# Performance work log

Measured on AMD Instinct MI355X. Metric: run time of the kernel, lower is better.

The kernel has to match this reference:

```python
import jax, jax.numpy as jnp
import numpy as np

N_NODES = 100000
IN_DIM = 64
OUT_DIM = 64
N_EDGES = 1600000


def _undirected_self_loops(edge_index, num_nodes):
    """Symmetrize, add self loops, coalesce (dedup+sort) like the torch module.
    edge_index is an integer constant, so we preprocess with numpy (no grads flow here).
    Returns (src, dst, w) where w are symmetric GCN normalization weights.
    """
    ei = np.asarray(edge_index, dtype=np.int64)
    loops = np.arange(num_nodes, dtype=np.int64)
    full_src = np.concatenate([ei[0], ei[1], loops])
    full_dst = np.concatenate([ei[1], ei[0], loops])
    keys = np.unique(full_src * num_nodes + full_dst)  # coalesce, sorted
    src = keys // num_nodes
    dst = keys % num_nodes
    deg = np.bincount(dst, minlength=num_nodes).clip(min=1)
    inv_sqrt = deg.astype(np.float32) ** -0.5
    w = inv_sqrt[src] * inv_sqrt[dst]
    return src, dst, w


def setup_inputs() -> dict:
    key = jax.random.key(0)
    kx, kw, kb, ke = jax.random.split(key, 4)
    x = jax.random.normal(kx, (N_NODES, IN_DIM), dtype=jnp.float32)
    # nn.Linear params: W (out, in), b (out,)
    W = jax.random.normal(kw, (OUT_DIM, IN_DIM), dtype=jnp.float32) / np.sqrt(IN_DIM)
    b = jax.random.normal(kb, (OUT_DIM,), dtype=jnp.float32) * 0.01
    edge_index = jax.random.randint(ke, (2, N_EDGES), 0, N_NODES, dtype=jnp.int64)
    return {"x": x, "edge_index": edge_index, "W": W, "b": b}


def reference(x, edge_index, W, b) -> jnp.ndarray:
    n = x.shape[0]
    src_np, dst_np, w_np = _undirected_self_loops(edge_index, n)
    src = jnp.asarray(src_np)
    dst = jnp.asarray(dst_np)
    w = jnp.asarray(w_np).astype(x.dtype)  # (E',)
    h = x @ W.T + b                         # (N, out_dim)
    msg = h[src] * w[:, None]               # gather + per-edge scale, (E', out_dim)
    out = jnp.zeros_like(h).at[dst].add(msg)  # scatter-add aggregation
    return out
```

## Files before the change

### kernel.cpp

```cpp
#include <hip/hip_runtime.h>
#include <hip/hip_bf16.h>
#include <stdint.h>

#define NN 100000
#define EE 1600000
#define CAP 128
#define NB 782
#define CAPB 5120
#define HTS 8192
#define EMPTY 0xFFFFFFFFu
#define BCHUNK 2048
#define GBIN 782
#define GLIN 1563

typedef float  fx4 __attribute__((ext_vector_type(4)));

__device__ __forceinline__ unsigned int mix32(unsigned int x){
  x ^= x >> 16; x *= 0x7feb352du;
  x ^= x >> 15; x *= 0x846ca68bu;
  x ^= x >> 16;
  return x;
}

extern "C" __global__ __launch_bounds__(256)
void k_prep(const float* __restrict__ x, const float* __restrict__ W,
            const float* __restrict__ bias, __hip_bfloat16* __restrict__ hb,
            const int* __restrict__ ei, int* __restrict__ bcnt,
            unsigned int* __restrict__ bbuf){
  __shared__ __align__(16) char sm[17920];
  const int tid = threadIdx.x;
  const int bid = blockIdx.x;
  const bool isbin = (bid < GBIN);
  const int sub = isbin ? bid : (bid - GBIN);

  if (!isbin){
    __hip_bfloat16 (*wt)[72] = reinterpret_cast<__hip_bfloat16(*)[72]>(sm);
    __hip_bfloat16 (*xs)[68] = reinterpret_cast<__hip_bfloat16(*)[68]>(sm + 9216);
    const int lane = tid & 63;
    const int wv   = tid >> 6;
    #pragma unroll
    for (int r = 0; r < 16; ++r){
      int i = r*4 + wv;
      wt[i][lane] = __float2bfloat16(W[lane*64 + i]);
    }
    const int nbase = sub * 64;
    #pragma unroll
    for (int r = 0; r < 4; ++r){
      int idx = r*256 + tid;
      int nl  = idx >> 4;
      int c4  = idx & 15;
      int n   = nbase + nl;
      float4 v = make_float4(0.f,0.f,0.f,0.f);
      if (n < NN) v = reinterpret_cast<const float4*>(x)[(size_t)n*16 + c4];
      xs[c4*4+0][nl] = __float2bfloat16(v.x);
      xs[c4*4+1][nl] = __float2bfloat16(v.y);
      xs[c4*4+2][nl] = __float2bfloat16(v.z);
      xs[c4*4+3][nl] = __float2bfloat16(v.w);
    }
    __syncthreads();

    const int og  = tid & 7;
    const int nl0 = (tid >> 3) * 2;
    float acc[2][8];
    #pragma unroll
    for (int t=0;t<2;++t){
      #pragma unroll
      for (int j=0;j<8;++j) acc[t][j]=0.f;
    }
    #pragma unroll 4
    for (int i=0;i<64;++i){
      uint4 wq = *reinterpret_cast<const uint4*>(&wt[i][og*8]);
      float w0 = __uint_as_float(wq.x << 16), w1 = __uint_as_float(wq.x & 0xFFFF0000u);
      float w2 = __uint_as_float(wq.y << 16), w3 = __uint_as_float(wq.y & 0xFFFF0000u);
      float w4 = __uint_as_float(wq.z << 16), w5 = __uint_as_float(wq.z & 0xFFFF0000u);
      float w6 = __uint_as_float(wq.w << 16), w7 = __uint_as_float(wq.w & 0xFFFF0000u);
      unsigned xv = *reinterpret_cast<const unsigned*>(&xs[i][nl0]);
      float x0 = __uint_as_float(xv << 16);
      float x1 = __uint_as_float(xv & 0xFFFF0000u);
      acc[0][0] += x0*w0; acc[0][1] += x0*w1; acc[0][2] += x0*w2; acc[0][3] += x0*w3;
      acc[0][4] += x0*w4; acc[0][5] += x0*w5; acc[0][6] += x0*w6; acc[0][7] += x0*w7;
      acc[1][0] += x1*w0; acc[1][1] += x1*w1; acc[1][2] += x1*w2; acc[1][3] += x1*w3;
      acc[1][4] += x1*w4; acc[1][5] += x1*w5; acc[1][6] += x1*w6; acc[1][7] += x1*w7;
    }
    float4 b0 = reinterpret_cast<const float4*>(bias)[og*2];
    float4 b1 = reinterpret_cast<const float4*>(bias)[og*2+1];
    float bb[8] = {b0.x,b0.y,b0.z,b0.w,b1.x,b1.y,b1.z,b1.w};
    #pragma unroll
    for (int t=0;t<2;++t){
      int n = nbase + nl0 + t;
      if (n < NN){
        union { uint4 u4; __hip_bfloat16 v[8]; } pk;
        #pragma unroll
        for (int j=0;j<8;++j) pk.v[j] = __float2bfloat16(acc[t][j] + bb[j]);
        reinterpret_cast<uint4*>(&hb[(size_t)n*64])[og] = pk.u4;
      }
    }
  } else {
    int* bcur  = reinterpret_cast<int*>(sm);
    int* bbase = bcur + NB;
    for (int i = tid; i < NB; i += 256) bcur[i] = 0;
    __syncthreads();
    const int e0 = sub * BCHUNK;
    const int4* ea4 = reinterpret_cast<const int4*>(ei);
    const int4* ec4 = reinterpret_cast<const int4*>(ei + EE);
    int4 A0, C0, A1, C1;
    unsigned P[8];
    {
      int idx0 = (e0 >> 2) + tid;
      int idx1 = idx0 + 256;
      if (idx0*4 < EE){ A0 = ea4[idx0]; C0 = ec4[idx0]; }
      else { A0 = make_int4(-1,-1,-1,-1); C0 = A0; }
      if (idx1*4 < EE){ A1 = ea4[idx1]; C1 = ec4[idx1]; }
      else { A1 = make_int4(-1,-1,-1,-1); C1 = A1; }
    }
#define RESV(a,c,slot) \
    if ((a) >= 0){ \
      unsigned p1 = (unsigned)atomicAdd(&bcur[(c) >> 7], 1); \
      unsigned p2 = (unsigned)atomicAdd(&bcur[(a) >> 7], 1); \
      P[slot] = p1 | (p2 << 16); \
    }
    RESV(A0.x, C0.x, 0) RESV(A0.y, C0.y, 1) RESV(A0.z, C0.z, 2) RESV(A0.w, C0.w, 3)
    RESV(A1.x, C1.x, 4) RESV(A1.y, C1.y, 5) RESV(A1.z, C1.z, 6) RESV(A1.w, C1.w, 7)
#undef RESV
    __syncthreads();
    for (int bk = tid; bk < NB; bk += 256){
      int hh = bcur[bk];
      bbase[bk] = hh ? atomicAdd(&bcnt[bk], hh) : 0;
    }
    __syncthreads();
#define PLACE(a,c,slot) \
    if ((a) >= 0){ \
      int b1 = (c) >> 7, b2 = (a) >> 7; \
      unsigned q1 = (unsigned)bbase[b1] + (P[slot] & 0xFFFFu); \
      unsigned q2 = (unsigned)bbase[b2] + (P[slot] >> 16); \
      if (q1 < CAPB) bbuf[(size_t)b1*CAPB + q1] = ((unsigned)(a) << 7) | (unsigned)((c) & 127); \
      if (q2 < CAPB) bbuf[(size_t)b2*CAPB + q2] = ((unsigned)(c) << 7) | (unsigned)((a) & 127); \
    }
    PLACE(A0.x, C0.x, 0) PLACE(A0.y, C0.y, 1) PLACE(A0.z, C0.z, 2) PLACE(A0.w, C0.w, 3)
    PLACE(A1.x, C1.x, 4) PLACE(A1.y, C1.y, 5) PLACE(A1.z, C1.z, 6) PLACE(A1.w, C1.w, 7)
#undef PLACE
  }
}

extern "C" __global__ __launch_bounds__(256)
void k_dedup(const int* __restrict__ bcnt, const unsigned int* __restrict__ bbuf,
             unsigned int* __restrict__ srclist, int* __restrict__ cnt,
             float* __restrict__ inv){
  __shared__ unsigned int HT[HTS];
  __shared__ int dcur[128];
  const int tid = threadIdx.x;
  const int b   = blockIdx.x;
  const int d0  = b << 7;
  uint4* HT4 = reinterpret_cast<uint4*>(HT);
  #pragma unroll
  for (int r = 0; r < 8; ++r) HT4[r*256 + tid] = make_uint4(EMPTY,EMPTY,EMPTY,EMPTY);
  if (tid < 128) dcur[tid] = 0;
  __syncthreads();

  int n = bcnt[b]; if (n > CAPB) n = CAPB;
  const unsigned int* buf = bbuf + (size_t)b * CAPB;
  for (int k = tid; k < n; k += 256){
    unsigned int pk  = buf[k];
    unsigned int idx = mix32(pk) & (HTS-1);
    for (;;){
      unsigned int prev = atomicCAS(&HT[idx], EMPTY, pk);
      if (prev == EMPTY || prev == pk) break;
      idx = (idx + 1) & (HTS-1);
    }
  }
  if (tid < 128 && d0 + tid < NN){
    unsigned int pk  = ((unsigned)(d0 + tid) << 7) | (unsigned)tid;
    unsigned int idx = mix32(pk) & (HTS-1);
    for (;;){
      unsigned int prev = atomicCAS(&HT[idx], EMPTY, pk);
      if (prev == EMPTY || prev == pk) break;
      idx = (idx + 1) & (HTS-1);
    }
  }
  __syncthreads();

  for (int i = tid; i < HTS; i += 256){
    unsigned int v = HT[i];
    if (v != EMPTY){
      int dl  = v & 127;
      int pos = atomicAdd(&dcur[dl], 1);
      if (pos < CAP) srclist[(size_t)(d0 + dl) * CAP + pos] = v >> 7;
    }
  }
  __syncthreads();
  if (tid < 128 && d0 + tid < NN){
    int c = dcur[tid];
    cnt[d0 + tid] = c;
    inv[d0 + tid] = rsqrtf((float)c);
  }
}

extern "C" __global__ __launch_bounds__(256)
void k_agg(const __hip_bfloat16* __restrict__ hb, const float* __restrict__ inv,
           const int* __restrict__ cnt, const unsigned int* __restrict__ srclist,
           float* __restrict__ out){
  __shared__ uint2 sv[4][CAP];
  const int wv   = threadIdx.x >> 6;
  const int lane = threadIdx.x & 63;
  const int g    = lane >> 4;
  const int pl   = lane & 15;
  const int d    = blockIdx.x*4 + wv;
  if (d >= NN) return;
  const unsigned int* reg = srclist + (size_t)d * CAP;
  int c = cnt[d]; if (c > CAP) c = CAP;
  const int cp = (c + 15) & ~15;

  if (lane < c){
    unsigned s = __builtin_nontemporal_load(reg + lane);
    sv[wv][lane] = make_uint2(s, __float_as_uint(inv[s]));
  }
  if (64 + lane < c){
    unsigned s = __builtin_nontemporal_load(reg + 64 + lane);
    sv[wv][64 + lane] = make_uint2(s, __float_as_uint(inv[s]));
  }
  { int p = c + lane; if (p < cp) sv[wv][p] = make_uint2(0u, 0u); }

  const char* hbase = (const char*)hb;
  const int   boff  = pl << 3;
  float4 acc[4];
  #pragma unroll
  for (int u=0;u<4;++u) acc[u] = make_float4(0.f,0.f,0.f,0.f);
  #pragma unroll 2
  for (int j = 0; j < cp; j += 16){
    #pragma unroll
    for (int u = 0; u < 4; ++u){
      uint2 e = sv[wv][j + 4*u + g];
      float w = __uint_as_float(e.y);
      uint2 hv = *reinterpret_cast<const uint2*>(hbase + ((size_t)e.x << 7) + boff);
      acc[u].x += w * __uint_as_float(hv.x << 16);
      acc[u].y += w * __uint_as_float(hv.x & 0xFFFF0000u);
      acc[u].z += w * __uint_as_float(hv.y << 16);
      acc[u].w += w * __uint_as_float(hv.y & 0xFFFF0000u);
    }
  }
  float4 r;
  r.x = (acc[0].x+acc[1].x)+(acc[2].x+acc[3].x);
  r.y = (acc[0].y+acc[1].y)+(acc[2].y+acc[3].y);
  r.z = (acc[0].z+acc[1].z)+(acc[2].z+acc[3].z);
  r.w = (acc[0].w+acc[1].w)+(acc[2].w+acc[3].w);
  r.x += __shfl_xor(r.x, 16); r.y += __shfl_xor(r.y, 16);
  r.z += __shfl_xor(r.z, 16); r.w += __shfl_xor(r.w, 16);
  r.x += __shfl_xor(r.x, 32); r.y += __shfl_xor(r.y, 32);
  r.z += __shfl_xor(r.z, 32); r.w += __shfl_xor(r.w, 32);
  if (g == 0){
    float iv = inv[d];
    fx4 o; o.x = r.x*iv; o.y = r.y*iv; o.z = r.z*iv; o.w = r.w*iv;
    __builtin_nontemporal_store(o, reinterpret_cast<fx4*>(&out[(size_t)d*64]) + pl);
  }
}

extern "C" void kernel_launch(void* const* d_in, const int* in_sizes, int n_in,
                              void* d_out, int out_size, void* d_ws, size_t ws_size,
                              hipStream_t stream){
  (void)in_sizes; (void)n_in; (void)out_size; (void)ws_size;
  const float* x  = (const float*)d_in[0];
  const int*   ei = (const int*)  d_in[1];
  const float* W  = (const float*)d_in[2];
  const float* b  = (const float*)d_in[3];
  float* out = (float*)d_out;

  char* ws = (char*)d_ws;
  __hip_bfloat16* hb      = (__hip_bfloat16*)ws;
  float*          inv     = (float*)(ws + 12800000);
  int*            cnt     = (int*)  (ws + 13200000);
  unsigned int*   srclist = (unsigned int*)(ws + 13600000);
  int*            bcnt    = (int*)  (ws + 64800000);
  unsigned int*   bbuf    = (unsigned int*)(ws + 64804096);

  (void)hipMemsetAsync(bcnt, 0, NB * 4, stream);

  k_prep  <<<GBIN + GLIN, 256, 0, stream>>>(x, W, b, hb, ei, bcnt, bbuf);
  k_dedup <<<NB, 256, 0, stream>>>(bcnt, bbuf, srclist, cnt, inv);
  k_agg   <<<(NN + 3)/4, 256, 0, stream>>>(hb, inv, cnt, srclist, out);
}
```

Measured before the change: 162.6 us.

## Replace global atomic bin offsets with per-block private bin segments

The binning phase now uses 98 larger blocks, each processing 16384 edges. Each block writes edges into its own private fixed-capacity segment per destination bin and records its own counts, so the global atomicAdd offset pass and the memset are no longer needed. The dedup kernel then walks the 98 segments per bin, one wave per segment. This removes global atomic contention and one block-wide barrier. In exchange, there are fewer binning blocks, a larger and sparser buffer, and a risk of silently dropping edges if a segment overflows its 96 slots.

```diff
diff --git a/kernel.cpp b/kernel.cpp
--- a/kernel.cpp
+++ b/kernel.cpp
@@ -6,14 +6,14 @@
 #define EE 1600000
 #define CAP 128
 #define NB 782
-#define CAPB 5120
 #define HTS 8192
 #define EMPTY 0xFFFFFFFFu
-#define BCHUNK 2048
-#define GBIN 782
+#define BCH 16384
+#define GBIN 98
+#define PRIV 96
 #define GLIN 1563
 
-typedef float  fx4 __attribute__((ext_vector_type(4)));
+typedef float fx4 __attribute__((ext_vector_type(4)));
 
 __device__ __forceinline__ unsigned int mix32(unsigned int x){
   x ^= x >> 16; x *= 0x7feb352du;
@@ -25,7 +25,7 @@
 extern "C" __global__ __launch_bounds__(256)
 void k_prep(const float* __restrict__ x, const float* __restrict__ W,
             const float* __restrict__ bias, __hip_bfloat16* __restrict__ hb,
-            const int* __restrict__ ei, int* __restrict__ bcnt,
+            const int* __restrict__ ei, int* __restrict__ gcnt,
             unsigned int* __restrict__ bbuf){
   __shared__ __align__(16) char sm[17920];
   const int tid = threadIdx.x;
@@ -96,58 +96,42 @@
       }
     }
   } else {
-    int* bcur  = reinterpret_cast<int*>(sm);
-    int* bbase = bcur + NB;
+    int* bcur = reinterpret_cast<int*>(sm);
     for (int i = tid; i < NB; i += 256) bcur[i] = 0;
     __syncthreads();
-    const int e0 = sub * BCHUNK;
+    const int base4 = (sub * BCH) >> 2;
     const int4* ea4 = reinterpret_cast<const int4*>(ei);
     const int4* ec4 = reinterpret_cast<const int4*>(ei + EE);
-    int4 A0, C0, A1, C1;
-    unsigned P[8];
-    {
-      int idx0 = (e0 >> 2) + tid;
-      int idx1 = idx0 + 256;
-      if (idx0*4 < EE){ A0 = ea4[idx0]; C0 = ec4[idx0]; }
-      else { A0 = make_int4(-1,-1,-1,-1); C0 = A0; }
-      if (idx1*4 < EE){ A1 = ea4[idx1]; C1 = ec4[idx1]; }
-      else { A1 = make_int4(-1,-1,-1,-1); C1 = A1; }
-    }
-#define RESV(a,c,slot) \
-    if ((a) >= 0){ \
-      unsigned p1 = (unsigned)atomicAdd(&bcur[(c) >> 7], 1); \
-      unsigned p2 = (unsigned)atomicAdd(&bcur[(a) >> 7], 1); \
-      P[slot] = p1 | (p2 << 16); \
-    }
-    RESV(A0.x, C0.x, 0) RESV(A0.y, C0.y, 1) RESV(A0.z, C0.z, 2) RESV(A0.w, C0.w, 3)
-    RESV(A1.x, C1.x, 4) RESV(A1.y, C1.y, 5) RESV(A1.z, C1.z, 6) RESV(A1.w, C1.w, 7)
-#undef RESV
+    #pragma unroll 1
+    for (int r = 0; r < 16; ++r){
+      int idx = base4 + r*256 + tid;
+      if (idx < (EE >> 2)){
+        int4 A = ea4[idx], C = ec4[idx];
+#define BIN1(a,c) { \
+        int b1 = (c) >> 7, b2 = (a) >> 7; \
+        int p1 = atomicAdd(&bcur[b1], 1); \
+        int p2 = atomicAdd(&bcur[b2], 1); \
+        if (p1 < PRIV) bbuf[((size_t)b1*GBIN + sub)*PRIV + p1] = ((unsigned)(a) << 7) | (unsigned)((c) & 127); \
+        if (p2 < PRIV) bbuf[((size_t)b2*GBIN + sub)*PRIV + p2] = ((unsigned)(c) << 7) | (unsigned)((a) & 127); }
+        BIN1(A.x, C.x) BIN1(A.y, C.y) BIN1(A.z, C.z) BIN1(A.w, C.w)
+#undef BIN1
+      }
+    }
     __syncthreads();
     for (int bk = tid; bk < NB; bk += 256){
-      int hh = bcur[bk];
-      bbase[bk] = hh ? atomicAdd(&bcnt[bk], hh) : 0;
-    }
-    __syncthreads();
-#define PLACE(a,c,slot) \
-    if ((a) >= 0){ \
-      int b1 = (c) >> 7, b2 = (a) >> 7; \
-      unsigned q1 = (unsigned)bbase[b1] + (P[slot] & 0xFFFFu); \
-      unsigned q2 = (unsigned)bbase[b2] + (P[slot] >> 16); \
-      if (q1 < CAPB) bbuf[(size_t)b1*CAPB + q1] = ((unsigned)(a) << 7) | (unsigned)((c) & 127); \
-      if (q2 < CAPB) bbuf[(size_t)b2*CAPB + q2] = ((unsigned)(c) << 7) | (unsigned)((a) & 127); \
-    }
-    PLACE(A0.x, C0.x, 0) PLACE(A0.y, C0.y, 1) PLACE(A0.z, C0.z, 2) PLACE(A0.w, C0.w, 3)
-    PLACE(A1.x, C1.x, 4) PLACE(A1.y, C1.y, 5) PLACE(A1.z, C1.z, 6) PLACE(A1.w, C1.w, 7)
-#undef PLACE
+      int c = bcur[bk];
+      gcnt[bk*GBIN + sub] = (c < PRIV) ? c : PRIV;
+    }
   }
 }
 
 extern "C" __global__ __launch_bounds__(256)
-void k_dedup(const int* __restrict__ bcnt, const unsigned int* __restrict__ bbuf,
+void k_dedup(const int* __restrict__ gcnt, const unsigned int* __restrict__ bbuf,
              unsigned int* __restrict__ srclist, int* __restrict__ cnt,
              float* __restrict__ inv){
   __shared__ unsigned int HT[HTS];
   __shared__ int dcur[128];
+  __shared__ int scnt[GBIN];
   const int tid = threadIdx.x;
   const int b   = blockIdx.x;
   const int d0  = b << 7;
@@ -155,17 +139,22 @@
   #pragma unroll
   for (int r = 0; r < 8; ++r) HT4[r*256 + tid] = make_uint4(EMPTY,EMPTY,EMPTY,EMPTY);
   if (tid < 128) dcur[tid] = 0;
+  if (tid < GBIN) scnt[tid] = gcnt[b*GBIN + tid];
   __syncthreads();
 
-  int n = bcnt[b]; if (n > CAPB) n = CAPB;
-  const unsigned int* buf = bbuf + (size_t)b * CAPB;
-  for (int k = tid; k < n; k += 256){
-    unsigned int pk  = buf[k];
-    unsigned int idx = mix32(pk) & (HTS-1);
-    for (;;){
-      unsigned int prev = atomicCAS(&HT[idx], EMPTY, pk);
-      if (prev == EMPTY || prev == pk) break;
-      idx = (idx + 1) & (HTS-1);
+  const int wv   = tid >> 6;
+  const int lane = tid & 63;
+  for (int seg = wv; seg < GBIN; seg += 4){
+    int m = scnt[seg];
+    const unsigned int* sb = bbuf + ((size_t)b*GBIN + seg)*PRIV;
+    for (int k = lane; k < m; k += 64){
+      unsigned int pk  = sb[k];
+      unsigned int idx = mix32(pk) & (HTS-1);
+      for (;;){
+        unsigned int prev = atomicCAS(&HT[idx], EMPTY, pk);
+        if (prev == EMPTY || prev == pk) break;
+        idx = (idx + 1) & (HTS-1);
+      }
     }
   }
   if (tid < 128 && d0 + tid < NN){
@@ -269,12 +258,10 @@
   float*          inv     = (float*)(ws + 12800000);
   int*            cnt     = (int*)  (ws + 13200000);
   unsigned int*   srclist = (unsigned int*)(ws + 13600000);
-  int*            bcnt    = (int*)  (ws + 64800000);
-  unsigned int*   bbuf    = (unsigned int*)(ws + 64804096);
-
-  (void)hipMemsetAsync(bcnt, 0, NB * 4, stream);
-
-  k_prep  <<<GBIN + GLIN, 256, 0, stream>>>(x, W, b, hb, ei, bcnt, bbuf);
-  k_dedup <<<NB, 256, 0, stream>>>(bcnt, bbuf, srclist, cnt, inv);
+  int*            gcnt    = (int*)  (ws + 64800000);
+  unsigned int*   bbuf    = (unsigned int*)(ws + 65200000);
+
+  k_prep  <<<GBIN + GLIN, 256, 0, stream>>>(x, W, b, hb, ei, gcnt, bbuf);
+  k_dedup <<<NB, 256, 0, stream>>>(gcnt, bbuf, srclist, cnt, inv);
   k_agg   <<<(NN + 3)/4, 256, 0, stream>>>(hb, inv, cnt, srclist, out);
 }
```

After: 145.5 us. -10.6%, faster.
